# Optimization experiments

Measured on AMD Instinct MI355X. Metric: run time of the kernel, lower is better.

Reference implementation:

```python
import jax, jax.numpy as jnp
import numpy as np

B, S = 4096, 256
D = 32  # output_size // 4


def setup_inputs() -> dict:
    key = jax.random.key(0)
    ks = jax.random.split(key, 32)
    # continuous features
    cont_p = jax.random.normal(ks[0], (B, S, 3), dtype=jnp.float32)
    cont_c = jax.random.normal(ks[1], (B, S, 2), dtype=jnp.float32)
    # categorical features, per-column vocab sizes from Embedding tables
    vocabs_p = [2, 2, 2, 11, 34]
    cat_p = jnp.stack([
        jax.random.randint(ks[2 + i], (B, S), 0, v, dtype=jnp.int32)
        for i, v in enumerate(vocabs_p)], axis=2)
    vocabs_c = [19, 31]
    cat_c = jnp.stack([
        jax.random.randint(ks[7 + i], (B, S), 0, v, dtype=jnp.int32)
        for i, v in enumerate(vocabs_c)], axis=2)
    lengths = jax.random.randint(ks[9], (B,), 1, S + 1, dtype=jnp.int32)

    def lin(k, fan_in, fan_out):
        bound = 1.0 / np.sqrt(fan_in)
        kw, kb = jax.random.split(k)
        w = jax.random.uniform(kw, (fan_in, fan_out), jnp.float32, -bound, bound)
        b = jax.random.uniform(kb, (fan_out,), jnp.float32, -bound, bound)
        return w, b

    w_p1, b_p1 = lin(ks[10], 3, D)
    w_p2, b_p2 = lin(ks[11], D, D)
    w_c1, b_c1 = lin(ks[12], 2, D)
    w_c2, b_c2 = lin(ks[13], D, D)
    emb_gender = jax.random.normal(ks[14], (2, D), dtype=jnp.float32)
    emb_korean = jax.random.normal(ks[15], (2, D), dtype=jnp.float32)
    emb_primary = jax.random.normal(ks[16], (2, D), dtype=jnp.float32)
    emb_job = jax.random.normal(ks[17], (11, D), dtype=jnp.float32)
    emb_rep = jax.random.normal(ks[18], (34, D), dtype=jnp.float32)
    emb_place = jax.random.normal(ks[19], (19, D), dtype=jnp.float32)
    emb_add = jax.random.normal(ks[20], (31, D), dtype=jnp.float32)
    w_fc1, b_fc1 = lin(ks[21], 128, 64)
    w_fc2, b_fc2 = lin(ks[22], 64, 2)

    return dict(cont_p=cont_p, cont_c=cont_c, cat_p=cat_p, cat_c=cat_c,
                lengths=lengths,
                w_p1=w_p1, b_p1=b_p1, w_p2=w_p2, b_p2=b_p2,
                w_c1=w_c1, b_c1=b_c1, w_c2=w_c2, b_c2=b_c2,
                emb_gender=emb_gender, emb_korean=emb_korean,
                emb_primary=emb_primary, emb_job=emb_job, emb_rep=emb_rep,
                emb_place=emb_place, emb_add=emb_add,
                w_fc1=w_fc1, b_fc1=b_fc1, w_fc2=w_fc2, b_fc2=b_fc2)


def reference(cont_p, cont_c, cat_p, cat_c, lengths,
              w_p1, b_p1, w_p2, b_p2, w_c1, b_c1, w_c2, b_c2,
              emb_gender, emb_korean, emb_primary, emb_job, emb_rep,
              emb_place, emb_add, w_fc1, b_fc1, w_fc2, b_fc2):
    # small per-token MLPs on continuous features -> [B,S,D]
    hp = jax.nn.relu(cont_p @ w_p1 + b_p1) @ w_p2 + b_p2
    hc = jax.nn.relu(cont_c @ w_c1 + b_c1) @ w_c2 + b_c2
    # multi-table embedding lookups, averaged per group -> [B,S,D]
    ep = (emb_gender[cat_p[:, :, 0]] + emb_korean[cat_p[:, :, 1]] +
          emb_primary[cat_p[:, :, 2]] + emb_job[cat_p[:, :, 3]] +
          emb_rep[cat_p[:, :, 4]]) / 5.0
    ec = (emb_place[cat_c[:, :, 0]] + emb_add[cat_c[:, :, 1]]) / 2.0
    # concat order matches torch: (cat_p, cat_c, cont_p, cont_c) -> [B,S,128]
    x = jnp.concatenate([ep, ec, hp, hc], axis=2)
    # ragged mean pool over first lengths[i] positions (masked segment mean)
    mask = (jnp.arange(x.shape[1])[None, :] < lengths[:, None])
    pooled = jnp.sum(x * mask[:, :, None], axis=1) / lengths[:, None].astype(x.dtype)
    # head: relu(fc1) -> relu(fc2); dropout p=0.0 is identity
    h = jax.nn.relu(pooled @ w_fc1 + b_fc1)
    return jax.nn.relu(h @ w_fc2 + b_fc2)
```

## Files before the change

kernel.cpp:

```cpp
#include <hip/hip_runtime.h>


#define BDIM 64

__global__ __launch_bounds__(BDIM, 4)
void mlpreg_kernel(const float* __restrict__ cont_p,
                   const float* __restrict__ cont_c,
                   const int* __restrict__ cat_p,
                   const int* __restrict__ cat_c,
                   const int* __restrict__ lengths,
                   const float* __restrict__ w_p1, const float* __restrict__ b_p1,
                   const float* __restrict__ w_p2, const float* __restrict__ b_p2,
                   const float* __restrict__ w_c1, const float* __restrict__ b_c1,
                   const float* __restrict__ w_c2, const float* __restrict__ b_c2,
                   const float* __restrict__ emb_g,  const float* __restrict__ emb_k,
                   const float* __restrict__ emb_pr, const float* __restrict__ emb_j,
                   const float* __restrict__ emb_r,  const float* __restrict__ emb_pl,
                   const float* __restrict__ emb_a,
                   const float* __restrict__ w_fc1, const float* __restrict__ b_fc1,
                   const float* __restrict__ w_fc2, const float* __restrict__ b_fc2,
                   float* __restrict__ out)
{
    constexpr int S = 256;
    __shared__ int   hist[96];
    __shared__ float sAcc[64];
    __shared__ float sPool[128];

    const int lane = threadIdx.x;
    const int b = blockIdx.x;
    const int ch = lane & 31, h = lane >> 5;

    int L = lengths[b]; L = (L < 1) ? 1 : (L > S ? S : L);
    const float Lf = (float)L, invL = 1.0f / Lf;

    hist[lane] = 0;
    if (lane < 32) hist[64 + lane] = 0;

    const float wp0 = w_p1[ch], wp1 = w_p1[32 + ch], wp2 = w_p1[64 + ch], bp = b_p1[ch];
    const float wc0 = w_c1[ch], wc1 = w_c1[32 + ch], bc = b_c1[ch];

    int sg = 0, sk = 0, sp = 0;
    {
        const int*  kp = cat_p + (size_t)b * (S * 5);
        const int2* kc = (const int2*)(cat_c + (size_t)b * (S * 2));
        #pragma unroll 2
        for (int t = lane; t < L; t += 64) {
            int v0 = kp[5 * t], v1 = kp[5 * t + 1], v2 = kp[5 * t + 2],
                v3 = kp[5 * t + 3], v4 = kp[5 * t + 4];
            int2 q = kc[t];
            sg += v0; sk += v1; sp += v2;
            atomicAdd(&hist[v3], 1);
            atomicAdd(&hist[11 + v4], 1);
            atomicAdd(&hist[45 + q.x], 1);
            atomicAdd(&hist[64 + q.y], 1);
        }
    }

    float aP = 0.f, aC = 0.f;
    {
        const float* tp = cont_p + (size_t)b * (S * 3);
        const float* tc = cont_c + (size_t)b * (S * 2);
        #pragma unroll 4
        for (int t = h; t < L; t += 2) {
            float c0 = tp[3 * t], c1 = tp[3 * t + 1], c2 = tp[3 * t + 2];
            float2 d2 = *(const float2*)&tc[2 * t];
            aP += fmaxf(fmaf(c0, wp0, fmaf(c1, wp1, fmaf(c2, wp2, bp))), 0.f);
            aC += fmaxf(fmaf(d2.x, wc0, fmaf(d2.y, wc1, bc)), 0.f);
        }
    }
    aP += __shfl_xor(aP, 32);
    aC += __shfl_xor(aC, 32);
    #pragma unroll
    for (int d = 32; d; d >>= 1) {
        sg += __shfl_xor(sg, d); sk += __shfl_xor(sk, d); sp += __shfl_xor(sp, d);
    }

    sAcc[lane] = (h ? aC : aP) * invL;
    __syncthreads();

    float A;
    {
        float fg = (float)sg, fk = (float)sk, fp = (float)sp;
        float g0 = emb_g[ch],  g1 = emb_g[32 + ch];
        float k0 = emb_k[ch],  k1 = emb_k[32 + ch];
        float p0 = emb_pr[ch], p1 = emb_pr[32 + ch];
        A = fmaf(Lf - fg, g0, fg * g1) + fmaf(Lf - fk, k0, fk * k1)
          + fmaf(Lf - fp, p0, fp * p1);
        A = h ? 0.f : A;
    }
    {
        const float* tA = h ? emb_pl : emb_j;
        const float* tB = h ? emb_a  : emb_r;
        const int nA = h ? 19 : 11;
        const int nT = h ? 50 : 45;
        const int hb = h ? 45 : 0;
        #pragma unroll 5
        for (int r = 0; r < nT; ++r) {
            const float* p = (r < nA) ? (tA + (r << 5)) : (tB + ((r - nA) << 5));
            A = fmaf((float)hist[hb + r], p[ch], A);
        }
        sPool[(h << 5) + ch] = A * (invL * (h ? 0.5f : 0.2f));
    }
    {
        const float* W2 = h ? w_c2 : w_p2;
        float v = (h ? b_c2 : b_p2)[ch];
        const float* acc = &sAcc[h << 5];
        #pragma unroll 8
        for (int k = 0; k < 32; ++k)
            v = fmaf(acc[k], W2[(k << 5) + ch], v);
        sPool[64 + (h << 5) + ch] = v;
    }
    __syncthreads();

    {
        float x = b_fc1[lane], y = 0.f;
        #pragma unroll 8
        for (int k = 0; k < 128; k += 4) {
            float4 u = *(const float4*)&sPool[k];
            float w0 = w_fc1[(size_t)(k    ) * 64 + lane];
            float w1 = w_fc1[(size_t)(k + 1) * 64 + lane];
            float w2 = w_fc1[(size_t)(k + 2) * 64 + lane];
            float w3 = w_fc1[(size_t)(k + 3) * 64 + lane];
            x = fmaf(u.x, w0, x); y = fmaf(u.y, w1, y);
            x = fmaf(u.z, w2, x); y = fmaf(u.w, w3, y);
        }
        float hv = fmaxf(x + y, 0.f);
        float q0 = hv * w_fc2[2 * lane], q1 = hv * w_fc2[2 * lane + 1];
        #pragma unroll
        for (int d = 32; d; d >>= 1) {
            q0 += __shfl_xor(q0, d); q1 += __shfl_xor(q1, d);
        }
        if (lane == 0) {
            float2 o2;
            o2.x = fmaxf(q0 + b_fc2[0], 0.f);
            o2.y = fmaxf(q1 + b_fc2[1], 0.f);
            *(float2*)&out[(size_t)b * 2] = o2;
        }
    }
}

extern "C" void kernel_launch(void* const* d_in, const int* in_sizes, int n_in,
                              void* d_out, int out_size, void* d_ws, size_t ws_size,
                              hipStream_t stream) {
    const float* cont_p = (const float*)d_in[0];
    const float* cont_c = (const float*)d_in[1];
    const int*   cat_p  = (const int*)d_in[2];
    const int*   cat_c  = (const int*)d_in[3];
    const int*   lens   = (const int*)d_in[4];
    const float* w_p1   = (const float*)d_in[5];
    const float* b_p1   = (const float*)d_in[6];
    const float* w_p2   = (const float*)d_in[7];
    const float* b_p2   = (const float*)d_in[8];
    const float* w_c1   = (const float*)d_in[9];
    const float* b_c1   = (const float*)d_in[10];
    const float* w_c2   = (const float*)d_in[11];
    const float* b_c2   = (const float*)d_in[12];
    const float* emb_g  = (const float*)d_in[13];
    const float* emb_k  = (const float*)d_in[14];
    const float* emb_pr = (const float*)d_in[15];
    const float* emb_j  = (const float*)d_in[16];
    const float* emb_r  = (const float*)d_in[17];
    const float* emb_pl = (const float*)d_in[18];
    const float* emb_a  = (const float*)d_in[19];
    const float* w_fc1  = (const float*)d_in[20];
    const float* b_fc1  = (const float*)d_in[21];
    const float* w_fc2  = (const float*)d_in[22];
    const float* b_fc2  = (const float*)d_in[23];
    float* out = (float*)d_out;

    hipLaunchKernelGGL(mlpreg_kernel, dim3(4096), dim3(BDIM), 0, stream,
                       cont_p, cont_c, cat_p, cat_c, lens,
                       w_p1, b_p1, w_p2, b_p2, w_c1, b_c1, w_c2, b_c2,
                       emb_g, emb_k, emb_pr, emb_j, emb_r, emb_pl, emb_a,
                       w_fc1, b_fc1, w_fc2, b_fc2, out);
}
```

Measured before the change: 155.2 us.

## Batch 8 rows per block and stage all weights in shared memory

```diff
diff --git a/kernel.cpp b/kernel.cpp
--- a/kernel.cpp
+++ b/kernel.cpp
@@ -1,7 +1,7 @@
 #include <hip/hip_runtime.h>
 
 
-#define BDIM 64
+#define BDIM 512
 
 __global__ __launch_bounds__(BDIM, 4)
 void mlpreg_kernel(const float* __restrict__ cont_p,
@@ -22,22 +22,63 @@
                    float* __restrict__ out)
 {
     constexpr int S = 256;
-    __shared__ int   hist[96];
-    __shared__ float sAcc[64];
-    __shared__ float sPool[128];
-
-    const int lane = threadIdx.x;
-    const int b = blockIdx.x;
-    const int ch = lane & 31, h = lane >> 5;
-
+    __shared__ float sWfc1[128 * 64];
+    __shared__ float sWp2[32 * 32];
+    __shared__ float sWc2[32 * 32];
+    __shared__ float sEmbT[95 * 32];
+    __shared__ float sEgkp[192];
+    __shared__ float sWp1[96], sBp1[32], sWc1[64], sBc1[32], sBp2[32], sBc2[32];
+    __shared__ float sBfc1[64], sWfc2[128], sBfc2[2];
+    __shared__ int   hist[8][96];
+    __shared__ float sAcc[8][64];
+    __shared__ float sPool[8][128];
+
+    const int tid  = threadIdx.x;
+    const int wid  = tid >> 6;
+    const int lane = tid & 63;
+    const int ch   = lane & 31, h = lane >> 5;
+
+    {
+        const float4* g = (const float4*)w_fc1;
+        float4* d = (float4*)sWfc1;
+        #pragma unroll
+        for (int i = tid; i < 2048; i += BDIM) d[i] = g[i];
+        for (int i = tid; i < 256; i += BDIM) ((float4*)sWp2)[i] = ((const float4*)w_p2)[i];
+        for (int i = tid; i < 256; i += BDIM) ((float4*)sWc2)[i] = ((const float4*)w_c2)[i];
+        float4* e = (float4*)sEmbT;
+        g = (const float4*)emb_j;
+        for (int i = tid; i < 88;  i += BDIM) e[i]       = g[i];
+        g = (const float4*)emb_r;
+        for (int i = tid; i < 272; i += BDIM) e[88 + i]  = g[i];
+        g = (const float4*)emb_pl;
+        for (int i = tid; i < 152; i += BDIM) e[360 + i] = g[i];
+        g = (const float4*)emb_a;
+        for (int i = tid; i < 248; i += BDIM) e[512 + i] = g[i];
+        if (tid < 64) {
+            sEgkp[tid]       = emb_g[tid];
+            sEgkp[64 + tid]  = emb_k[tid];
+            sEgkp[128 + tid] = emb_pr[tid];
+            sWc1[tid]  = w_c1[tid];
+            sBfc1[tid] = b_fc1[tid];
+        }
+        if (tid < 96)  sWp1[tid]  = w_p1[tid];
+        if (tid < 128) sWfc2[tid] = w_fc2[tid];
+        if (tid < 32) {
+            sBp1[tid] = b_p1[tid]; sBc1[tid] = b_c1[tid];
+            sBp2[tid] = b_p2[tid]; sBc2[tid] = b_c2[tid];
+        }
+        if (tid < 2) sBfc2[tid] = b_fc2[tid];
+    }
+    hist[wid][lane] = 0;
+    if (lane < 32) hist[wid][64 + lane] = 0;
+    __syncthreads();
+
+    const int b = blockIdx.x * 8 + wid;
     int L = lengths[b]; L = (L < 1) ? 1 : (L > S ? S : L);
     const float Lf = (float)L, invL = 1.0f / Lf;
 
-    hist[lane] = 0;
-    if (lane < 32) hist[64 + lane] = 0;
-
-    const float wp0 = w_p1[ch], wp1 = w_p1[32 + ch], wp2 = w_p1[64 + ch], bp = b_p1[ch];
-    const float wc0 = w_c1[ch], wc1 = w_c1[32 + ch], bc = b_c1[ch];
+    const float wp0 = sWp1[ch], wp1 = sWp1[32 + ch], wp2 = sWp1[64 + ch], bp = sBp1[ch];
+    const float wc0 = sWc1[ch], wc1 = sWc1[32 + ch], bc = sBc1[ch];
 
     int sg = 0, sk = 0, sp = 0;
     {
@@ -49,10 +90,10 @@
                 v3 = kp[5 * t + 3], v4 = kp[5 * t + 4];
             int2 q = kc[t];
             sg += v0; sk += v1; sp += v2;
-            atomicAdd(&hist[v3], 1);
-            atomicAdd(&hist[11 + v4], 1);
-            atomicAdd(&hist[45 + q.x], 1);
-            atomicAdd(&hist[64 + q.y], 1);
+            atomicAdd(&hist[wid][v3], 1);
+            atomicAdd(&hist[wid][11 + v4], 1);
+            atomicAdd(&hist[wid][45 + q.x], 1);
+            atomicAdd(&hist[wid][64 + q.y], 1);
         }
     }
 
@@ -74,66 +115,57 @@
     for (int d = 32; d; d >>= 1) {
         sg += __shfl_xor(sg, d); sk += __shfl_xor(sk, d); sp += __shfl_xor(sp, d);
     }
-
-    sAcc[lane] = (h ? aC : aP) * invL;
+    sAcc[wid][lane] = (h ? aC : aP) * invL;
     __syncthreads();
 
     float A;
     {
         float fg = (float)sg, fk = (float)sk, fp = (float)sp;
-        float g0 = emb_g[ch],  g1 = emb_g[32 + ch];
-        float k0 = emb_k[ch],  k1 = emb_k[32 + ch];
-        float p0 = emb_pr[ch], p1 = emb_pr[32 + ch];
+        float g0 = sEgkp[ch],       g1 = sEgkp[32 + ch];
+        float k0 = sEgkp[64 + ch],  k1 = sEgkp[96 + ch];
+        float p0 = sEgkp[128 + ch], p1 = sEgkp[160 + ch];
         A = fmaf(Lf - fg, g0, fg * g1) + fmaf(Lf - fk, k0, fk * k1)
           + fmaf(Lf - fp, p0, fp * p1);
         A = h ? 0.f : A;
     }
     {
-        const float* tA = h ? emb_pl : emb_j;
-        const float* tB = h ? emb_a  : emb_r;
-        const int nA = h ? 19 : 11;
         const int nT = h ? 50 : 45;
         const int hb = h ? 45 : 0;
+        const int* hrow = hist[wid];
         #pragma unroll 5
-        for (int r = 0; r < nT; ++r) {
-            const float* p = (r < nA) ? (tA + (r << 5)) : (tB + ((r - nA) << 5));
-            A = fmaf((float)hist[hb + r], p[ch], A);
-        }
-        sPool[(h << 5) + ch] = A * (invL * (h ? 0.5f : 0.2f));
-    }
-    {
-        const float* W2 = h ? w_c2 : w_p2;
-        float v = (h ? b_c2 : b_p2)[ch];
-        const float* acc = &sAcc[h << 5];
+        for (int r = 0; r < nT; ++r)
+            A = fmaf((float)hrow[hb + r], sEmbT[(hb + r) * 32 + ch], A);
+        sPool[wid][(h << 5) + ch] = A * (invL * (h ? 0.5f : 0.2f));
+    }
+    {
+        const float* W2 = h ? sWc2 : sWp2;
+        float v = h ? sBc2[ch] : sBp2[ch];
+        const float* acc = &sAcc[wid][h << 5];
         #pragma unroll 8
         for (int k = 0; k < 32; ++k)
             v = fmaf(acc[k], W2[(k << 5) + ch], v);
-        sPool[64 + (h << 5) + ch] = v;
+        sPool[wid][64 + (h << 5) + ch] = v;
     }
     __syncthreads();
 
     {
-        float x = b_fc1[lane], y = 0.f;
+        float x = sBfc1[lane], y = 0.f;
         #pragma unroll 8
-        for (int k = 0; k < 128; k += 4) {
-            float4 u = *(const float4*)&sPool[k];
-            float w0 = w_fc1[(size_t)(k    ) * 64 + lane];
-            float w1 = w_fc1[(size_t)(k + 1) * 64 + lane];
-            float w2 = w_fc1[(size_t)(k + 2) * 64 + lane];
-            float w3 = w_fc1[(size_t)(k + 3) * 64 + lane];
-            x = fmaf(u.x, w0, x); y = fmaf(u.y, w1, y);
-            x = fmaf(u.z, w2, x); y = fmaf(u.w, w3, y);
+        for (int k = 0; k < 128; k += 2) {
+            float2 u = *(const float2*)&sPool[wid][k];
+            x = fmaf(u.x, sWfc1[k * 64 + lane], x);
+            y = fmaf(u.y, sWfc1[(k + 1) * 64 + lane], y);
         }
         float hv = fmaxf(x + y, 0.f);
-        float q0 = hv * w_fc2[2 * lane], q1 = hv * w_fc2[2 * lane + 1];
+        float q0 = hv * sWfc2[2 * lane], q1 = hv * sWfc2[2 * lane + 1];
         #pragma unroll
         for (int d = 32; d; d >>= 1) {
             q0 += __shfl_xor(q0, d); q1 += __shfl_xor(q1, d);
         }
         if (lane == 0) {
             float2 o2;
-            o2.x = fmaxf(q0 + b_fc2[0], 0.f);
-            o2.y = fmaxf(q1 + b_fc2[1], 0.f);
+            o2.x = fmaxf(q0 + sBfc2[0], 0.f);
+            o2.y = fmaxf(q1 + sBfc2[1], 0.f);
             *(float2*)&out[(size_t)b * 2] = o2;
         }
     }
@@ -168,7 +200,7 @@
     const float* b_fc2  = (const float*)d_in[23];
     float* out = (float*)d_out;
 
-    hipLaunchKernelGGL(mlpreg_kernel, dim3(4096), dim3(BDIM), 0, stream,
+    hipLaunchKernelGGL(mlpreg_kernel, dim3(512), dim3(BDIM), 0, stream,
                        cont_p, cont_c, cat_p, cat_c, lens,
                        w_p1, b_p1, w_p2, b_p2, w_c1, b_c1, w_c2, b_c2,
                        emb_g, emb_k, emb_pr, emb_j, emb_r, emb_pl, emb_a,
```

Measured after the change: 154.3 us. About the same (-0.6%).

## Batch 16 rows per 512-thread block and stage inputs and fc1 weights in LDS

Applied to the files above, without the earlier changes.

```diff
diff --git a/kernel.cpp b/kernel.cpp
--- a/kernel.cpp
+++ b/kernel.cpp
@@ -1,9 +1,9 @@
 #include <hip/hip_runtime.h>
 
 
-#define BDIM 64
-
-__global__ __launch_bounds__(BDIM, 4)
+#define BDIM 512
+
+__global__ __launch_bounds__(BDIM, 1)
 void mlpreg_kernel(const float* __restrict__ cont_p,
                    const float* __restrict__ cont_c,
                    const int* __restrict__ cat_p,
@@ -22,71 +22,124 @@
                    float* __restrict__ out)
 {
     constexpr int S = 256;
-    __shared__ int   hist[96];
-    __shared__ float sAcc[64];
-    __shared__ float sPool[128];
-
-    const int lane = threadIdx.x;
-    const int b = blockIdx.x;
-    const int ch = lane & 31, h = lane >> 5;
-
-    int L = lengths[b]; L = (L < 1) ? 1 : (L > S ? S : L);
-    const float Lf = (float)L, invL = 1.0f / Lf;
-
-    hist[lane] = 0;
-    if (lane < 32) hist[64 + lane] = 0;
+    __shared__ float sPc[16 * 768];
+    __shared__ float sCc[16 * 512];
+    __shared__ float sW1[128 * 64];
+    __shared__ float sAcc[16][64];
+    __shared__ float sPB[16 * 128];
+
+    const int tid  = threadIdx.x;
+    const int wid  = tid >> 6;
+    const int lane = tid & 63;
+    const int ch   = lane & 31, h = lane >> 5;
+    const int lr0  = wid << 1;
+    const int b0   = blockIdx.x * 16 + lr0, b1 = b0 + 1;
+
+    int L0 = lengths[b0]; L0 = (L0 < 1) ? 1 : (L0 > S ? S : L0);
+    int L1 = lengths[b1]; L1 = (L1 < 1) ? 1 : (L1 > S ? S : L1);
+    const float L0f = (float)L0, L1f = (float)L1;
+    const float invL0 = 1.0f / L0f, invL1 = 1.0f / L1f;
 
     const float wp0 = w_p1[ch], wp1 = w_p1[32 + ch], wp2 = w_p1[64 + ch], bp = b_p1[ch];
     const float wc0 = w_c1[ch], wc1 = w_c1[32 + ch], bc = b_c1[ch];
-
-    int sg = 0, sk = 0, sp = 0;
-    {
-        const int*  kp = cat_p + (size_t)b * (S * 5);
-        const int2* kc = (const int2*)(cat_c + (size_t)b * (S * 2));
+    const float eg0 = emb_g[ch],  eg1 = emb_g[32 + ch];
+    const float ek0 = emb_k[ch],  ek1 = emb_k[32 + ch];
+    const float er0 = emb_pr[ch], er1 = emb_pr[32 + ch];
+    const float bias2 = h ? b_c2[ch] : b_p2[ch];
+    const float bf1 = b_fc1[lane];
+    const float2 wf2 = *(const float2*)&w_fc2[2 * lane];
+    const float bq0 = b_fc2[0], bq1 = b_fc2[1];
+
+    {
+        const float4* gp0 = (const float4*)(cont_p + (size_t)b0 * 768);
+        const float4* gp1 = (const float4*)(cont_p + (size_t)b1 * 768);
+        const float4* gc0 = (const float4*)(cont_c + (size_t)b0 * 512);
+        const float4* gc1 = (const float4*)(cont_c + (size_t)b1 * 512);
+        float4* dp0 = (float4*)(sPc + lr0 * 768);
+        float4* dp1 = (float4*)(sPc + (lr0 + 1) * 768);
+        float4* dc0 = (float4*)(sCc + lr0 * 512);
+        float4* dc1 = (float4*)(sCc + (lr0 + 1) * 512);
+        const int n0 = (3 * L0 + 3) >> 2, n1 = (3 * L1 + 3) >> 2;
+        const int m0 = (L0 + 1) >> 1,     m1 = (L1 + 1) >> 1;
+        for (int i = lane; i < n0; i += 64) dp0[i] = gp0[i];
+        for (int i = lane; i < n1; i += 64) dp1[i] = gp1[i];
+        for (int i = lane; i < m0; i += 64) dc0[i] = gc0[i];
+        for (int i = lane; i < m1; i += 64) dc1[i] = gc1[i];
+    }
+    {
+        const float4* gw = (const float4*)w_fc1;
+        float4* dw = (float4*)sW1;
+        #pragma unroll
+        for (int i = tid; i < 2048; i += BDIM) dw[i] = gw[i];
+    }
+    int* hist0 = (int*)(sPB + lr0 * 128);
+    int* hist1 = (int*)(sPB + (lr0 + 1) * 128);
+    hist0[lane] = 0; hist1[lane] = 0;
+    if (lane < 32) { hist0[64 + lane] = 0; hist1[64 + lane] = 0; }
+
+    int sg0 = 0, sk0 = 0, sp0 = 0, sg1 = 0, sk1 = 0, sp1 = 0;
+    {
+        const int*  kp0 = cat_p + (size_t)b0 * (S * 5);
+        const int*  kp1 = cat_p + (size_t)b1 * (S * 5);
+        const int2* kc0 = (const int2*)(cat_c + (size_t)b0 * (S * 2));
+        const int2* kc1 = (const int2*)(cat_c + (size_t)b1 * (S * 2));
         #pragma unroll 2
-        for (int t = lane; t < L; t += 64) {
-            int v0 = kp[5 * t], v1 = kp[5 * t + 1], v2 = kp[5 * t + 2],
-                v3 = kp[5 * t + 3], v4 = kp[5 * t + 4];
-            int2 q = kc[t];
-            sg += v0; sk += v1; sp += v2;
-            atomicAdd(&hist[v3], 1);
-            atomicAdd(&hist[11 + v4], 1);
-            atomicAdd(&hist[45 + q.x], 1);
-            atomicAdd(&hist[64 + q.y], 1);
-        }
-    }
-
-    float aP = 0.f, aC = 0.f;
-    {
-        const float* tp = cont_p + (size_t)b * (S * 3);
-        const float* tc = cont_c + (size_t)b * (S * 2);
+        for (int t = lane; t < L0; t += 64) {
+            int v0 = kp0[5 * t], v1 = kp0[5 * t + 1], v2 = kp0[5 * t + 2],
+                v3 = kp0[5 * t + 3], v4 = kp0[5 * t + 4];
+            int2 q = kc0[t];
+            sg0 += v0; sk0 += v1; sp0 += v2;
+            atomicAdd(&hist0[v3], 1);
+            atomicAdd(&hist0[11 + v4], 1);
+            atomicAdd(&hist0[45 + q.x], 1);
+            atomicAdd(&hist0[64 + q.y], 1);
+        }
+        #pragma unroll 2
+        for (int t = lane; t < L1; t += 64) {
+            int v0 = kp1[5 * t], v1 = kp1[5 * t + 1], v2 = kp1[5 * t + 2],
+                v3 = kp1[5 * t + 3], v4 = kp1[5 * t + 4];
+            int2 q = kc1[t];
+            sg1 += v0; sk1 += v1; sp1 += v2;
+            atomicAdd(&hist1[v3], 1);
+            atomicAdd(&hist1[11 + v4], 1);
+            atomicAdd(&hist1[45 + q.x], 1);
+            atomicAdd(&hist1[64 + q.y], 1);
+        }
+    }
+    #pragma unroll
+    for (int d = 32; d; d >>= 1) {
+        sg0 += __shfl_xor(sg0, d); sk0 += __shfl_xor(sk0, d); sp0 += __shfl_xor(sp0, d);
+        sg1 += __shfl_xor(sg1, d); sk1 += __shfl_xor(sk1, d); sp1 += __shfl_xor(sp1, d);
+    }
+    __syncthreads();
+
+    {
+        const int   lr   = lr0 + h;
+        const int   Lr   = h ? L1 : L0;
+        const float invr = h ? invL1 : invL0;
+        const float* tp = sPc + lr * 768;
+        const float* tc = sCc + lr * 512;
+        float aP = 0.f, aC = 0.f;
         #pragma unroll 4
-        for (int t = h; t < L; t += 2) {
+        for (int t = 0; t < Lr; ++t) {
             float c0 = tp[3 * t], c1 = tp[3 * t + 1], c2 = tp[3 * t + 2];
             float2 d2 = *(const float2*)&tc[2 * t];
             aP += fmaxf(fmaf(c0, wp0, fmaf(c1, wp1, fmaf(c2, wp2, bp))), 0.f);
             aC += fmaxf(fmaf(d2.x, wc0, fmaf(d2.y, wc1, bc)), 0.f);
         }
-    }
-    aP += __shfl_xor(aP, 32);
-    aC += __shfl_xor(aC, 32);
-    #pragma unroll
-    for (int d = 32; d; d >>= 1) {
-        sg += __shfl_xor(sg, d); sk += __shfl_xor(sk, d); sp += __shfl_xor(sp, d);
-    }
-
-    sAcc[lane] = (h ? aC : aP) * invL;
-    __syncthreads();
-
-    float A;
-    {
-        float fg = (float)sg, fk = (float)sk, fp = (float)sp;
-        float g0 = emb_g[ch],  g1 = emb_g[32 + ch];
-        float k0 = emb_k[ch],  k1 = emb_k[32 + ch];
-        float p0 = emb_pr[ch], p1 = emb_pr[32 + ch];
-        A = fmaf(Lf - fg, g0, fg * g1) + fmaf(Lf - fk, k0, fk * k1)
-          + fmaf(Lf - fp, p0, fp * p1);
-        A = h ? 0.f : A;
+        sAcc[lr][ch]      = aP * invr;
+        sAcc[lr][32 + ch] = aC * invr;
+    }
+
+    float A0, A1;
+    {
+        float fg0 = (float)sg0, fk0 = (float)sk0, fp0 = (float)sp0;
+        float fg1 = (float)sg1, fk1 = (float)sk1, fp1 = (float)sp1;
+        A0 = fmaf(L0f - fg0, eg0, fg0 * eg1) + fmaf(L0f - fk0, ek0, fk0 * ek1)
+           + fmaf(L0f - fp0, er0, fp0 * er1);
+        A1 = fmaf(L1f - fg1, eg0, fg1 * eg1) + fmaf(L1f - fk1, ek0, fk1 * ek1)
+           + fmaf(L1f - fp1, er0, fp1 * er1);
+        if (h) { A0 = 0.f; A1 = 0.f; }
     }
     {
         const float* tA = h ? emb_pl : emb_j;
@@ -97,44 +150,58 @@
         #pragma unroll 5
         for (int r = 0; r < nT; ++r) {
             const float* p = (r < nA) ? (tA + (r << 5)) : (tB + ((r - nA) << 5));
-            A = fmaf((float)hist[hb + r], p[ch], A);
-        }
-        sPool[(h << 5) + ch] = A * (invL * (h ? 0.5f : 0.2f));
+            float w = p[ch];
+            A0 = fmaf((float)hist0[hb + r], w, A0);
+            A1 = fmaf((float)hist1[hb + r], w, A1);
+        }
+        const float sc = h ? 0.5f : 0.2f;
+        sPB[lr0 * 128 + (h << 5) + ch]       = A0 * (invL0 * sc);
+        sPB[(lr0 + 1) * 128 + (h << 5) + ch] = A1 * (invL1 * sc);
     }
     {
         const float* W2 = h ? w_c2 : w_p2;
-        float v = (h ? b_c2 : b_p2)[ch];
-        const float* acc = &sAcc[h << 5];
+        const float* a0 = &sAcc[lr0][h << 5];
+        const float* a1 = &sAcc[lr0 + 1][h << 5];
+        float v0 = bias2, v1 = bias2;
         #pragma unroll 8
-        for (int k = 0; k < 32; ++k)
-            v = fmaf(acc[k], W2[(k << 5) + ch], v);
-        sPool[64 + (h << 5) + ch] = v;
-    }
-    __syncthreads();
-
-    {
-        float x = b_fc1[lane], y = 0.f;
+        for (int k = 0; k < 32; ++k) {
+            float w = W2[(k << 5) + ch];
+            v0 = fmaf(a0[k], w, v0);
+            v1 = fmaf(a1[k], w, v1);
+        }
+        sPB[lr0 * 128 + 64 + (h << 5) + ch]       = v0;
+        sPB[(lr0 + 1) * 128 + 64 + (h << 5) + ch] = v1;
+    }
+
+    {
+        const float* P0 = sPB + lr0 * 128;
+        const float* P1 = P0 + 128;
+        float x0 = bf1, y0 = 0.f, x1 = bf1, y1 = 0.f;
         #pragma unroll 8
-        for (int k = 0; k < 128; k += 4) {
-            float4 u = *(const float4*)&sPool[k];
-            float w0 = w_fc1[(size_t)(k    ) * 64 + lane];
-            float w1 = w_fc1[(size_t)(k + 1) * 64 + lane];
-            float w2 = w_fc1[(size_t)(k + 2) * 64 + lane];
-            float w3 = w_fc1[(size_t)(k + 3) * 64 + lane];
-            x = fmaf(u.x, w0, x); y = fmaf(u.y, w1, y);
-            x = fmaf(u.z, w2, x); y = fmaf(u.w, w3, y);
-        }
-        float hv = fmaxf(x + y, 0.f);
-        float q0 = hv * w_fc2[2 * lane], q1 = hv * w_fc2[2 * lane + 1];
+        for (int k = 0; k < 128; k += 2) {
+            float w0 = sW1[k * 64 + lane];
+            float w1 = sW1[(k + 1) * 64 + lane];
+            float2 u0 = *(const float2*)&P0[k];
+            float2 u1 = *(const float2*)&P1[k];
+            x0 = fmaf(u0.x, w0, x0); y0 = fmaf(u0.y, w1, y0);
+            x1 = fmaf(u1.x, w0, x1); y1 = fmaf(u1.y, w1, y1);
+        }
+        float h0v = fmaxf(x0 + y0, 0.f);
+        float h1v = fmaxf(x1 + y1, 0.f);
+        float q00 = h0v * wf2.x, q01 = h0v * wf2.y;
+        float q10 = h1v * wf2.x, q11 = h1v * wf2.y;
         #pragma unroll
         for (int d = 32; d; d >>= 1) {
-            q0 += __shfl_xor(q0, d); q1 += __shfl_xor(q1, d);
+            q00 += __shfl_xor(q00, d); q01 += __shfl_xor(q01, d);
+            q10 += __shfl_xor(q10, d); q11 += __shfl_xor(q11, d);
         }
         if (lane == 0) {
-            float2 o2;
-            o2.x = fmaxf(q0 + b_fc2[0], 0.f);
-            o2.y = fmaxf(q1 + b_fc2[1], 0.f);
-            *(float2*)&out[(size_t)b * 2] = o2;
+            float4 o4;
+            o4.x = fmaxf(q00 + bq0, 0.f);
+            o4.y = fmaxf(q01 + bq1, 0.f);
+            o4.z = fmaxf(q10 + bq0, 0.f);
+            o4.w = fmaxf(q11 + bq1, 0.f);
+            *(float4*)&out[(size_t)b0 * 2] = o4;
         }
     }
 }
@@ -168,7 +235,7 @@
     const float* b_fc2  = (const float*)d_in[23];
     float* out = (float*)d_out;
 
-    hipLaunchKernelGGL(mlpreg_kernel, dim3(4096), dim3(BDIM), 0, stream,
+    hipLaunchKernelGGL(mlpreg_kernel, dim3(256), dim3(BDIM), 0, stream,
                        cont_p, cont_c, cat_p, cat_c, lens,
                        w_p1, b_p1, w_p2, b_p2, w_c1, b_c1, w_c2, b_c2,
                        emb_g, emb_k, emb_pr, emb_j, emb_r, emb_pl, emb_a,
```

Measured after the change: 143.2 us. 7.7% less time.

## Stage per-row inputs into LDS with async global_load_lds and vectorized parsing

Applied to the files above, without the earlier changes.

```diff
diff --git a/kernel.cpp b/kernel.cpp
--- a/kernel.cpp
+++ b/kernel.cpp
@@ -3,7 +3,13 @@
 
 #define BDIM 64
 
-__global__ __launch_bounds__(BDIM, 4)
+__device__ __forceinline__ void gld16(const void* g, void* l) {
+    __builtin_amdgcn_global_load_lds((__attribute__((address_space(1))) void*)g,
+                                     (__attribute__((address_space(3))) void*)l,
+                                     16, 0, 0);
+}
+
+__global__ __launch_bounds__(BDIM)
 void mlpreg_kernel(const float* __restrict__ cont_p,
                    const float* __restrict__ cont_c,
                    const int* __restrict__ cat_p,
@@ -22,70 +28,143 @@
                    float* __restrict__ out)
 {
     constexpr int S = 256;
-    __shared__ int   hist[96];
-    __shared__ float sAcc[64];
-    __shared__ float sPool[128];
+    __shared__ __align__(16) float sBuf[2560];
+    float* sPc  = sBuf;
+    float* sCc  = sBuf + 768;
+    int*   sKp  = (int*)(sBuf + 1280);
+    int*   hist = (int*)sBuf;
+    float* sAcc = sBuf + 768;
+    float* sPool = sBuf + 832;
 
     const int lane = threadIdx.x;
+    const int ch = lane & 31, h = lane >> 5;
     const int b = blockIdx.x;
-    const int ch = lane & 31, h = lane >> 5;
 
     int L = lengths[b]; L = (L < 1) ? 1 : (L > S ? S : L);
     const float Lf = (float)L, invL = 1.0f / Lf;
 
+    {
+        const char* gp = (const char*)(cont_p + (size_t)b * 768);
+        const char* gc = (const char*)(cont_c + (size_t)b * 512);
+        const char* gk = (const char*)(cat_p + (size_t)b * 1280);
+        const int lo = 16 * lane;
+        const int bP = 12 * L, bC = 8 * L, bK = 20 * L;
+        gld16(gp + lo, (char*)sPc);
+        if (1024 < bP) gld16(gp + 1024 + lo, (char*)sPc + 1024);
+        if (2048 < bP) gld16(gp + 2048 + lo, (char*)sPc + 2048);
+        gld16(gc + lo, (char*)sCc);
+        if (1024 < bC) gld16(gc + 1024 + lo, (char*)sCc + 1024);
+        #pragma unroll
+        for (int j = 0; j < 5; ++j)
+            if (1024 * j < bK) gld16(gk + 1024 * j + lo, (char*)sKp + 1024 * j);
+    }
+    const int limc = 2 * L;
+    const int4* KC = (const int4*)(cat_c + (size_t)b * 512);
+    int4 qc0, qc1;
+    const bool hc0 = (4 * lane < limc), hc1 = (256 + 4 * lane < limc);
+    if (hc0) qc0 = KC[lane];
+    if (hc1) qc1 = KC[lane + 64];
+
+    const float wp0 = w_p1[ch], wp1 = w_p1[32 + ch], wp2 = w_p1[64 + ch], bp = b_p1[ch];
+    const float wc0 = w_c1[ch], wc1 = w_c1[32 + ch], bc = b_c1[ch];
+    const float eg0 = emb_g[ch],  eg1 = emb_g[32 + ch];
+    const float ek0 = emb_k[ch],  ek1 = emb_k[32 + ch];
+    const float er0 = emb_pr[ch], er1 = emb_pr[32 + ch];
+    const float bias2 = h ? b_c2[ch] : b_p2[ch];
+    const float bf1 = b_fc1[lane];
+    const float2 wf2 = *(const float2*)&w_fc2[2 * lane];
+    const float bq0 = b_fc2[0], bq1 = b_fc2[1];
+
+    __syncthreads();
+
+    float aP = 0.f, aC = 0.f;
+    {
+        const int gf = L >> 2;
+        const int gh = (gf + 1) >> 1;
+        const float4* tp4 = (const float4*)sPc;
+        const float4* tc4 = (const float4*)sCc;
+        #pragma unroll 4
+        for (int i = 0; i < gh; ++i) {
+            const int g = h ? gh + i : i;
+            if (g < gf) {
+                float4 a  = tp4[3 * g], bb = tp4[3 * g + 1], cc = tp4[3 * g + 2];
+                float4 d  = tc4[2 * g], ee = tc4[2 * g + 1];
+                float p0 = fmaxf(fmaf(a.x,  wp0, fmaf(a.y,  wp1, fmaf(a.z,  wp2, bp))), 0.f);
+                float p1 = fmaxf(fmaf(a.w,  wp0, fmaf(bb.x, wp1, fmaf(bb.y, wp2, bp))), 0.f);
+                float p2 = fmaxf(fmaf(bb.z, wp0, fmaf(bb.w, wp1, fmaf(cc.x, wp2, bp))), 0.f);
+                float p3 = fmaxf(fmaf(cc.y, wp0, fmaf(cc.z, wp1, fmaf(cc.w, wp2, bp))), 0.f);
+                aP += (p0 + p1) + (p2 + p3);
+                float q0 = fmaxf(fmaf(d.x,  wc0, fmaf(d.y,  wc1, bc)), 0.f);
+                float q1 = fmaxf(fmaf(d.z,  wc0, fmaf(d.w,  wc1, bc)), 0.f);
+                float q2 = fmaxf(fmaf(ee.x, wc0, fmaf(ee.y, wc1, bc)), 0.f);
+                float q3 = fmaxf(fmaf(ee.z, wc0, fmaf(ee.w, wc1, bc)), 0.f);
+                aC += (q0 + q1) + (q2 + q3);
+            }
+        }
+        const int rem = L & 3;
+        if (h == 0 && rem) {
+            const float* tp = sPc + 12 * gf;
+            const float* tc = sCc + 8 * gf;
+            for (int r = 0; r < rem; ++r) {
+                aP += fmaxf(fmaf(tp[3*r], wp0, fmaf(tp[3*r+1], wp1, fmaf(tp[3*r+2], wp2, bp))), 0.f);
+                aC += fmaxf(fmaf(tc[2*r], wc0, fmaf(tc[2*r+1], wc1, bc)), 0.f);
+            }
+        }
+        aP += __shfl_xor(aP, 32);
+        aC += __shfl_xor(aC, 32);
+        sAcc[lane] = (h ? aC : aP) * invL;
+    }
+    __syncthreads();
+
     hist[lane] = 0;
     if (lane < 32) hist[64 + lane] = 0;
 
-    const float wp0 = w_p1[ch], wp1 = w_p1[32 + ch], wp2 = w_p1[64 + ch], bp = b_p1[ch];
-    const float wc0 = w_c1[ch], wc1 = w_c1[32 + ch], bc = b_c1[ch];
-
     int sg = 0, sk = 0, sp = 0;
     {
-        const int*  kp = cat_p + (size_t)b * (S * 5);
-        const int2* kc = (const int2*)(cat_c + (size_t)b * (S * 2));
-        #pragma unroll 2
-        for (int t = lane; t < L; t += 64) {
-            int v0 = kp[5 * t], v1 = kp[5 * t + 1], v2 = kp[5 * t + 2],
-                v3 = kp[5 * t + 3], v4 = kp[5 * t + 4];
-            int2 q = kc[t];
-            sg += v0; sk += v1; sp += v2;
-            atomicAdd(&hist[v3], 1);
-            atomicAdd(&hist[11 + v4], 1);
-            atomicAdd(&hist[45 + q.x], 1);
-            atomicAdd(&hist[64 + q.y], 1);
-        }
-    }
-
-    float aP = 0.f, aC = 0.f;
-    {
-        const float* tp = cont_p + (size_t)b * (S * 3);
-        const float* tc = cont_c + (size_t)b * (S * 2);
-        #pragma unroll 4
-        for (int t = h; t < L; t += 2) {
-            float c0 = tp[3 * t], c1 = tp[3 * t + 1], c2 = tp[3 * t + 2];
-            float2 d2 = *(const float2*)&tc[2 * t];
-            aP += fmaxf(fmaf(c0, wp0, fmaf(c1, wp1, fmaf(c2, wp2, bp))), 0.f);
-            aC += fmaxf(fmaf(d2.x, wc0, fmaf(d2.y, wc1, bc)), 0.f);
-        }
-    }
-    aP += __shfl_xor(aP, 32);
-    aC += __shfl_xor(aC, 32);
+        const int limp = 5 * L;
+        const int m0 = (lane << 2) % 5;
+        #pragma unroll
+        for (int j = 0; j < 5; ++j) {
+            if (256 * j < limp) {
+                int4 v4 = ((const int4*)sKp)[lane + 64 * j];
+                const int base = 4 * lane + 256 * j;
+                int mj = m0 + j; if (mj >= 5) mj -= 5;
+                const int v[4] = {v4.x, v4.y, v4.z, v4.w};
+                #pragma unroll
+                for (int c = 0; c < 4; ++c) {
+                    int f = mj + c; if (f >= 5) f -= 5;
+                    const bool val = (base + c) < limp;
+                    const int vv = v[c];
+                    sg += (val && f == 0) ? vv : 0;
+                    sk += (val && f == 1) ? vv : 0;
+                    sp += (val && f == 2) ? vv : 0;
+                    if (val && f >= 3) atomicAdd(&hist[(f == 4 ? 11 : 0) + vv], 1);
+                }
+            }
+        }
+        if (hc0) {
+            atomicAdd(&hist[45 + qc0.x], 1);
+            if (4 * lane + 1 < limc) atomicAdd(&hist[64 + qc0.y], 1);
+            if (4 * lane + 2 < limc) atomicAdd(&hist[45 + qc0.z], 1);
+            if (4 * lane + 3 < limc) atomicAdd(&hist[64 + qc0.w], 1);
+        }
+        if (hc1) {
+            atomicAdd(&hist[45 + qc1.x], 1);
+            if (257 + 4 * lane < limc) atomicAdd(&hist[64 + qc1.y], 1);
+            if (258 + 4 * lane < limc) atomicAdd(&hist[45 + qc1.z], 1);
+            if (259 + 4 * lane < limc) atomicAdd(&hist[64 + qc1.w], 1);
+        }
+    }
     #pragma unroll
     for (int d = 32; d; d >>= 1) {
         sg += __shfl_xor(sg, d); sk += __shfl_xor(sk, d); sp += __shfl_xor(sp, d);
     }
 
-    sAcc[lane] = (h ? aC : aP) * invL;
-    __syncthreads();
-
     float A;
     {
         float fg = (float)sg, fk = (float)sk, fp = (float)sp;
-        float g0 = emb_g[ch],  g1 = emb_g[32 + ch];
-        float k0 = emb_k[ch],  k1 = emb_k[32 + ch];
-        float p0 = emb_pr[ch], p1 = emb_pr[32 + ch];
-        A = fmaf(Lf - fg, g0, fg * g1) + fmaf(Lf - fk, k0, fk * k1)
-          + fmaf(Lf - fp, p0, fp * p1);
+        A = fmaf(Lf - fg, eg0, fg * eg1) + fmaf(Lf - fk, ek0, fk * ek1)
+          + fmaf(Lf - fp, er0, fp * er1);
         A = h ? 0.f : A;
     }
     {
@@ -103,37 +182,33 @@
     }
     {
         const float* W2 = h ? w_c2 : w_p2;
-        float v = (h ? b_c2 : b_p2)[ch];
-        const float* acc = &sAcc[h << 5];
+        const float* acc = sAcc + (h << 5);
+        float v = bias2;
         #pragma unroll 8
         for (int k = 0; k < 32; ++k)
             v = fmaf(acc[k], W2[(k << 5) + ch], v);
         sPool[64 + (h << 5) + ch] = v;
     }
-    __syncthreads();
-
-    {
-        float x = b_fc1[lane], y = 0.f;
+
+    {
+        float x = bf1, y = 0.f;
         #pragma unroll 8
-        for (int k = 0; k < 128; k += 4) {
-            float4 u = *(const float4*)&sPool[k];
-            float w0 = w_fc1[(size_t)(k    ) * 64 + lane];
+        for (int k = 0; k < 128; k += 2) {
+            float w0 = w_fc1[(size_t)k * 64 + lane];
             float w1 = w_fc1[(size_t)(k + 1) * 64 + lane];
-            float w2 = w_fc1[(size_t)(k + 2) * 64 + lane];
-            float w3 = w_fc1[(size_t)(k + 3) * 64 + lane];
+            float2 u = *(const float2*)&sPool[k];
             x = fmaf(u.x, w0, x); y = fmaf(u.y, w1, y);
-            x = fmaf(u.z, w2, x); y = fmaf(u.w, w3, y);
         }
         float hv = fmaxf(x + y, 0.f);
-        float q0 = hv * w_fc2[2 * lane], q1 = hv * w_fc2[2 * lane + 1];
+        float q0 = hv * wf2.x, q1 = hv * wf2.y;
         #pragma unroll
         for (int d = 32; d; d >>= 1) {
             q0 += __shfl_xor(q0, d); q1 += __shfl_xor(q1, d);
         }
         if (lane == 0) {
             float2 o2;
-            o2.x = fmaxf(q0 + b_fc2[0], 0.f);
-            o2.y = fmaxf(q1 + b_fc2[1], 0.f);
+            o2.x = fmaxf(q0 + bq0, 0.f);
+            o2.y = fmaxf(q1 + bq1, 0.f);
             *(float2*)&out[(size_t)b * 2] = o2;
         }
     }
```

Result: faster. 141.1 us (-9.1%).
